# Kernel tuning notes

Hardware: AMD Instinct MI355X
Metric: run time of the kernel (lower is better)

The kernel has to match this reference:

```python
import jax, jax.numpy as jnp
import numpy as np

DIM = 1024
NUM_HEADS = 16
HEAD_DIM = DIM // NUM_HEADS
SCALE = HEAD_DIM ** -0.5


def setup_inputs() -> dict:
    key = jax.random.key(0)
    k1, k2, k3 = jax.random.split(key, 3)
    B, N = 4, 2048
    x = jax.random.normal(k1, (B, N, DIM), dtype=jnp.float32)
    W_qkv = jax.random.normal(k2, (DIM, 3 * DIM), dtype=jnp.float32) * (DIM ** -0.5)
    b_qkv = jnp.zeros((3 * DIM,), dtype=jnp.float32)
    W_proj = jax.random.normal(k3, (DIM, DIM), dtype=jnp.float32) * (DIM ** -0.5)
    b_proj = jnp.zeros((DIM,), dtype=jnp.float32)
    return {"x": x, "W_qkv": W_qkv, "b_qkv": b_qkv, "W_proj": W_proj, "b_proj": b_proj}


def reference(x, W_qkv, b_qkv, W_proj, b_proj):
    B, N, D = x.shape
    qkv = x @ W_qkv + b_qkv                       # [B, N, 3D]
    qkv = qkv.reshape(B, N, 3, NUM_HEADS, HEAD_DIM)
    qkv = jnp.transpose(qkv, (2, 0, 3, 1, 4))     # [3, B, H, N, hd]
    q, k, v = qkv[0], qkv[1], qkv[2]
    attn = jnp.einsum('bhnd,bhmd->bhnm', q, k) * SCALE
    attn = jax.nn.softmax(attn, axis=-1)
    out = jnp.einsum('bhnm,bhmd->bhnd', attn, v)  # [B, H, N, hd]
    out = jnp.transpose(out, (0, 2, 1, 3)).reshape(B, N, D)
    return out @ W_proj + b_proj
```

## Files before the change

kernel.cpp:

```cpp
#include <hip/hip_runtime.h>
#include <hip/hip_bf16.h>

#define BATCH 4
#define SEQ   2048
#define DIM   1024
#define NHEAD 16
#define HDIM  64
#define ROWS  (BATCH * SEQ)
#define LS    68
#define GLS   68
#define QSCALE 0.18033688011f

typedef __bf16 bf16x8 __attribute__((ext_vector_type(8)));
typedef float  f32x4  __attribute__((ext_vector_type(4)));
typedef float  f32x16 __attribute__((ext_vector_type(16)));

static __device__ __forceinline__ uint pack2(float a, float b) {
    ushort ua = __builtin_bit_cast(ushort, (__bf16)a);
    ushort ub = __builtin_bit_cast(ushort, (__bf16)b);
    return (uint)ua | ((uint)ub << 16);
}
#define PLSWAP(a, b) asm volatile("v_permlane32_swap_b32 %0, %1" : "+v"(a), "+v"(b))

__global__ __launch_bounds__(256)
void convert_bf16_kernel(const float* __restrict__ in, ushort* __restrict__ out, int n8) {
    int stride = gridDim.x * blockDim.x;
    for (int i = blockIdx.x * blockDim.x + threadIdx.x; i < n8; i += stride) {
        float4 a = ((const float4*)in)[2 * i];
        float4 b = ((const float4*)in)[2 * i + 1];
        ushort u[8];
        u[0] = __builtin_bit_cast(ushort, (__bf16)a.x);
        u[1] = __builtin_bit_cast(ushort, (__bf16)a.y);
        u[2] = __builtin_bit_cast(ushort, (__bf16)a.z);
        u[3] = __builtin_bit_cast(ushort, (__bf16)a.w);
        u[4] = __builtin_bit_cast(ushort, (__bf16)b.x);
        u[5] = __builtin_bit_cast(ushort, (__bf16)b.y);
        u[6] = __builtin_bit_cast(ushort, (__bf16)b.z);
        u[7] = __builtin_bit_cast(ushort, (__bf16)b.w);
        ((uint4*)out)[i] = *(uint4*)u;
    }
}

__global__ __launch_bounds__(256)
void transpose_bf16_kernel(const float* __restrict__ W, ushort* __restrict__ Wt,
                           int K, int N) {
    __shared__ float tile[32][33];
    const int tx = threadIdx.x, ty = threadIdx.y;
    const int n0 = blockIdx.x * 32, k0 = blockIdx.y * 32;
#pragma unroll
    for (int i = 0; i < 4; ++i)
        tile[ty + 8 * i][tx] = W[(long)(k0 + ty + 8 * i) * N + n0 + tx];
    __syncthreads();
#pragma unroll
    for (int i = 0; i < 4; ++i) {
        float v = tile[tx][ty + 8 * i];
        Wt[(long)(n0 + ty + 8 * i) * K + k0 + tx] = __builtin_bit_cast(ushort, (__bf16)v);
    }
}

__global__ __launch_bounds__(256)
void gemm_mfma_kernel(const ushort* __restrict__ A, const ushort* __restrict__ Bt,
                      const float* __restrict__ bias,
                      int M, int N, int K, int mode,
                      __hip_bfloat16* __restrict__ Qb,
                      __hip_bfloat16* __restrict__ Kb,
                      __hip_bfloat16* __restrict__ Vb,
                      float* __restrict__ Cout) {
    const int t  = threadIdx.x;
    const int w  = t >> 6;
    const int l  = t & 63;
    const int c  = l & 15;
    const int g  = l >> 4;
    const int wr = w >> 1, wc = w & 1;
    const int row0 = blockIdx.y * 128;
    const int col0 = blockIdx.x * 128;

    __shared__ ushort As[128][GLS];
    __shared__ ushort Bs[128][GLS];

    const int sr = t >> 3;
    const int sa = t & 7;

    f32x4 acc[4][4];
#pragma unroll
    for (int i = 0; i < 4; ++i)
#pragma unroll
        for (int j = 0; j < 4; ++j) acc[i][j] = (f32x4){0.f, 0.f, 0.f, 0.f};

    for (int k0 = 0; k0 < K; k0 += 64) {
        __syncthreads();
#pragma unroll
        for (int i = 0; i < 4; ++i) {
            int row = i * 32 + sr;
            uint4 a = *(const uint4*)(A + (size_t)(row0 + row) * K + k0 + 8 * sa);
            *(uint2*)&As[row][8 * sa]     = make_uint2(a.x, a.y);
            *(uint2*)&As[row][8 * sa + 4] = make_uint2(a.z, a.w);
            uint4 b = *(const uint4*)(Bt + (size_t)(col0 + row) * K + k0 + 8 * sa);
            *(uint2*)&Bs[row][8 * sa]     = make_uint2(b.x, b.y);
            *(uint2*)&Bs[row][8 * sa + 4] = make_uint2(b.z, b.w);
        }
        __syncthreads();

#pragma unroll
        for (int ks = 0; ks < 2; ++ks) {
            bf16x8 am[4], bn[4];
#pragma unroll
            for (int mt = 0; mt < 4; ++mt) {
                uint2 a0 = *(const uint2*)&As[wr * 64 + mt * 16 + c][ks * 32 + 8 * g];
                uint2 a1 = *(const uint2*)&As[wr * 64 + mt * 16 + c][ks * 32 + 8 * g + 4];
                am[mt] = __builtin_bit_cast(bf16x8, make_uint4(a0.x, a0.y, a1.x, a1.y));
            }
#pragma unroll
            for (int nt = 0; nt < 4; ++nt) {
                uint2 b0 = *(const uint2*)&Bs[wc * 64 + nt * 16 + c][ks * 32 + 8 * g];
                uint2 b1 = *(const uint2*)&Bs[wc * 64 + nt * 16 + c][ks * 32 + 8 * g + 4];
                bn[nt] = __builtin_bit_cast(bf16x8, make_uint4(b0.x, b0.y, b1.x, b1.y));
            }
#pragma unroll
            for (int mt = 0; mt < 4; ++mt)
#pragma unroll
                for (int nt = 0; nt < 4; ++nt)
                    acc[mt][nt] = __builtin_amdgcn_mfma_f32_16x16x32_bf16(
                        am[mt], bn[nt], acc[mt][nt], 0, 0, 0);
        }
    }

    float bv[4];
#pragma unroll
    for (int nt = 0; nt < 4; ++nt) bv[nt] = bias[col0 + wc * 64 + nt * 16 + c];

#pragma unroll
    for (int mt = 0; mt < 4; ++mt) {
#pragma unroll
        for (int r = 0; r < 4; ++r) {
            int grow = row0 + wr * 64 + mt * 16 + 4 * g + r;
#pragma unroll
            for (int nt = 0; nt < 4; ++nt) {
                int gcol = col0 + wc * 64 + nt * 16 + c;
                float v = acc[mt][nt][r] + bv[nt];
                if (mode == 0) {
                    int s = gcol >> 10;
                    int hc = gcol & 1023;
                    int h = hc >> 6, d = hc & 63;
                    int bi = grow >> 11, n = grow & 2047;
                    size_t off = ((size_t)(bi * NHEAD + h) * SEQ + n) * HDIM + d;
                    if (s == 0) v *= QSCALE;
                    __hip_bfloat16 hb = __float2bfloat16(v);
                    if (s == 0)      Qb[off] = hb;
                    else if (s == 1) Kb[off] = hb;
                    else             Vb[off] = hb;
                } else {
                    Cout[(size_t)grow * N + gcol] = v;
                }
            }
        }
    }
}

__global__ __launch_bounds__(256)
void attn_mfma2_kernel(const ushort* __restrict__ Qg,
                       const ushort* __restrict__ Kg,
                       const ushort* __restrict__ Vg,
                       ushort* __restrict__ O) {
    const int id  = blockIdx.x;
    const int bh  = (id & 7) * 8 + ((id >> 3) & 7);
    const int qt  = id >> 6;
    const int t   = threadIdx.x;
    const int w   = t >> 6, l = t & 63;
    const int lo5 = l & 31, hi = l >> 5;
    const size_t base = (size_t)bh * SEQ * HDIM;
    const int q0  = qt * 128 + w * 32;

    __shared__ ushort Ks[2][64 * LS];
    __shared__ ushort Vt[2][64 * LS];

    bf16x8 qf[4];
    {
        const ushort* qrow = Qg + base + (size_t)(q0 + lo5) * HDIM + 8 * hi;
#pragma unroll
        for (int db = 0; db < 4; ++db)
            qf[db] = __builtin_bit_cast(bf16x8, *(const uint4*)(qrow + 16 * db));
    }

    const int ksr = t & 63, kch = t >> 6;
    const int vkp = t & 31, vcg = t >> 5;
    const ushort* Kptr = Kg + base + (size_t)ksr * HDIM + 16 * kch;
    const ushort* Vptr = Vg + base + (size_t)(2 * vkp) * HDIM + 8 * vcg;

    auto stageK = [&](int buf, uint4 a, uint4 b) {
        ushort* p = &Ks[buf][ksr * LS + 16 * kch];
        *(uint2*)(p)      = make_uint2(a.x, a.y);
        *(uint2*)(p + 4)  = make_uint2(a.z, a.w);
        *(uint2*)(p + 8)  = make_uint2(b.x, b.y);
        *(uint2*)(p + 12) = make_uint2(b.z, b.w);
    };
    auto stageV = [&](int buf, uint4 a, uint4 b) {
        const uint* pa = (const uint*)&a;
        const uint* pb = (const uint*)&b;
#pragma unroll
        for (int e = 0; e < 8; ++e) {
            uint sel = (e & 1) ? 0x07060302u : 0x05040100u;
            uint packed = __builtin_amdgcn_perm(pb[e >> 1], pa[e >> 1], sel);
            *(uint*)&Vt[buf][(8 * vcg + e) * LS + 2 * vkp] = packed;
        }
    };

    uint4 kr0, kr1, vr0, vr1;
    kr0 = *(const uint4*)(Kptr);
    kr1 = *(const uint4*)(Kptr + 8);
    vr0 = *(const uint4*)(Vptr);
    vr1 = *(const uint4*)(Vptr + HDIM);
    stageK(0, kr0, kr1);
    stageV(0, vr0, vr1);
    {
        const size_t off = (size_t)64 * HDIM;
        kr0 = *(const uint4*)(Kptr + off);
        kr1 = *(const uint4*)(Kptr + off + 8);
        vr0 = *(const uint4*)(Vptr + off);
        vr1 = *(const uint4*)(Vptr + off + HDIM);
    }
    __syncthreads();

    f32x16 o0, o1;
#pragma unroll
    for (int r = 0; r < 16; ++r) { o0[r] = 0.f; o1[r] = 0.f; }
    float m0 = -1e30f, ll = 0.f;

    for (int kt = 0; kt < 32; ++kt) {
        const int cur = kt & 1;
        if (kt < 31) {
            stageK(cur ^ 1, kr0, kr1);
            stageV(cur ^ 1, vr0, vr1);
        }
        if (kt < 30) {
            const size_t off = (size_t)(kt + 2) * 64 * HDIM;
            kr0 = *(const uint4*)(Kptr + off);
            kr1 = *(const uint4*)(Kptr + off + 8);
            vr0 = *(const uint4*)(Vptr + off);
            vr1 = *(const uint4*)(Vptr + off + HDIM);
        }

        f32x16 s[2];
        __builtin_amdgcn_s_setprio(1);
#pragma unroll
        for (int kb = 0; kb < 2; ++kb) {
            f32x16 acc;
#pragma unroll
            for (int r = 0; r < 16; ++r) acc[r] = 0.f;
#pragma unroll
            for (int db = 0; db < 4; ++db) {
                const ushort* ap = &Ks[cur][(kb * 32 + lo5) * LS + 16 * db + 8 * hi];
                uint2 a0 = *(const uint2*)(ap);
                uint2 a1 = *(const uint2*)(ap + 4);
                bf16x8 af = __builtin_bit_cast(bf16x8, make_uint4(a0.x, a0.y, a1.x, a1.y));
                acc = __builtin_amdgcn_mfma_f32_32x32x16_bf16(af, qf[db], acc, 0, 0, 0);
            }
            s[kb] = acc;
        }
        __builtin_amdgcn_s_setprio(0);

        float c0 = s[0][0], c1 = s[0][1];
#pragma unroll
        for (int r = 2; r < 16; r += 2) {
            c0 = fmaxf(fmaxf(c0, s[0][r]), s[0][r + 1]);
            c1 = fmaxf(fmaxf(c1, s[1][r]), s[1][r + 1]);
        }
        c0 = fmaxf(fmaxf(c0, s[1][0]), s[1][1]);
        float pmax = fmaxf(c0, c1);
        pmax = fmaxf(pmax, __shfl_xor(pmax, 32, 64));

        if (!__all(pmax <= m0 + 8.f)) {
            float mn = fmaxf(m0, pmax);
            float corr = __builtin_amdgcn_exp2f(m0 - mn);
#pragma unroll
            for (int r = 0; r < 16; ++r) { o0[r] *= corr; o1[r] *= corr; }
            ll *= corr;
            m0 = mn;
        }
        float a0 = 0.f, a1 = 0.f, a2 = 0.f, a3 = 0.f;
#pragma unroll
        for (int r = 0; r < 16; r += 2) {
            float p0 = __builtin_amdgcn_exp2f(s[0][r]     - m0); s[0][r]     = p0; a0 += p0;
            float p1 = __builtin_amdgcn_exp2f(s[0][r + 1] - m0); s[0][r + 1] = p1; a1 += p1;
            float p2 = __builtin_amdgcn_exp2f(s[1][r]     - m0); s[1][r]     = p2; a2 += p2;
            float p3 = __builtin_amdgcn_exp2f(s[1][r + 1] - m0); s[1][r + 1] = p3; a3 += p3;
        }
        float rs = (a0 + a1) + (a2 + a3);
        rs += __shfl_xor(rs, 32, 64);
        ll += rs;

        bf16x8 pbf[4];
#pragma unroll
        for (int kb = 0; kb < 2; ++kb)
#pragma unroll
            for (int kk = 0; kk < 2; ++kk) {
                const int b0 = kk * 8;
                uint w0 = pack2(s[kb][b0 + 0], s[kb][b0 + 1]);
                uint w1 = pack2(s[kb][b0 + 2], s[kb][b0 + 3]);
                uint w2 = pack2(s[kb][b0 + 4], s[kb][b0 + 5]);
                uint w3 = pack2(s[kb][b0 + 6], s[kb][b0 + 7]);
                PLSWAP(w0, w2);
                PLSWAP(w1, w3);
                pbf[kb * 2 + kk] = __builtin_bit_cast(bf16x8, make_uint4(w0, w1, w2, w3));
            }

        __builtin_amdgcn_s_setprio(1);
#pragma unroll
        for (int kb = 0; kb < 2; ++kb)
#pragma unroll
            for (int kk = 0; kk < 2; ++kk) {
                const int kcol = kb * 32 + kk * 16 + 8 * hi;
                const ushort* vp0 = &Vt[cur][lo5 * LS + kcol];
                uint2 v0 = *(const uint2*)(vp0);
                uint2 v1 = *(const uint2*)(vp0 + 4);
                bf16x8 vf0 = __builtin_bit_cast(bf16x8, make_uint4(v0.x, v0.y, v1.x, v1.y));
                o0 = __builtin_amdgcn_mfma_f32_32x32x16_bf16(vf0, pbf[kb * 2 + kk], o0, 0, 0, 0);
                const ushort* vp1 = vp0 + 32 * LS;
                uint2 v2 = *(const uint2*)(vp1);
                uint2 v3 = *(const uint2*)(vp1 + 4);
                bf16x8 vf1 = __builtin_bit_cast(bf16x8, make_uint4(v2.x, v2.y, v3.x, v3.y));
                o1 = __builtin_amdgcn_mfma_f32_32x32x16_bf16(vf1, pbf[kb * 2 + kk], o1, 0, 0, 0);
            }
        __builtin_amdgcn_s_setprio(0);

        __syncthreads();
    }

    const float inv = 1.f / ll;
    const int b = bh >> 4, h = bh & 15;
    ushort* orow = O + (size_t)(b * SEQ + q0 + lo5) * DIM + h * HDIM;
#pragma unroll
    for (int j = 0; j < 4; ++j) {
        uint2 st;
        st.x = pack2(o0[4 * j + 0] * inv, o0[4 * j + 1] * inv);
        st.y = pack2(o0[4 * j + 2] * inv, o0[4 * j + 3] * inv);
        *(uint2*)(orow + 8 * j + 4 * hi) = st;
        st.x = pack2(o1[4 * j + 0] * inv, o1[4 * j + 1] * inv);
        st.y = pack2(o1[4 * j + 2] * inv, o1[4 * j + 3] * inv);
        *(uint2*)(orow + 32 + 8 * j + 4 * hi) = st;
    }
}

extern "C" void kernel_launch(void* const* d_in, const int* in_sizes, int n_in,
                              void* d_out, int out_size, void* d_ws, size_t ws_size,
                              hipStream_t stream) {
    const float* x      = (const float*)d_in[0];
    const float* W_qkv  = (const float*)d_in[1];
    const float* b_qkv  = (const float*)d_in[2];
    const float* W_proj = (const float*)d_in[3];
    const float* b_proj = (const float*)d_in[4];
    float* out = (float*)d_out;

    const size_t qkv_elems = (size_t)BATCH * NHEAD * SEQ * HDIM;
    char* ws = (char*)d_ws;
    ushort* xb      = (ushort*)ws;
    ushort* Wqkv_t  = (ushort*)(ws + qkv_elems * 2);
    ushort* Wproj_t = (ushort*)(ws + qkv_elems * 2 + (size_t)DIM * 3 * DIM * 2);
    char*   ws2     = ws + qkv_elems * 2 + (size_t)DIM * 3 * DIM * 2 + (size_t)DIM * DIM * 2;
    __hip_bfloat16* Qb = (__hip_bfloat16*)ws2;
    __hip_bfloat16* Kb = (__hip_bfloat16*)(ws2 + qkv_elems * 2);
    __hip_bfloat16* Vb = (__hip_bfloat16*)(ws2 + qkv_elems * 4);
    ushort* attnout = xb;

    convert_bf16_kernel<<<2048, 256, 0, stream>>>(x, xb, ROWS * DIM / 8);
    transpose_bf16_kernel<<<dim3(3 * DIM / 32, DIM / 32), dim3(32, 8), 0, stream>>>(
        W_qkv, Wqkv_t, DIM, 3 * DIM);
    transpose_bf16_kernel<<<dim3(DIM / 32, DIM / 32), dim3(32, 8), 0, stream>>>(
        W_proj, Wproj_t, DIM, DIM);

    gemm_mfma_kernel<<<dim3(3 * DIM / 128, ROWS / 128), 256, 0, stream>>>(
        xb, Wqkv_t, b_qkv, ROWS, 3 * DIM, DIM, 0, Qb, Kb, Vb, nullptr);

    attn_mfma2_kernel<<<dim3(1024), 256, 0, stream>>>(
        (const ushort*)Qb, (const ushort*)Kb, (const ushort*)Vb, attnout);

    gemm_mfma_kernel<<<dim3(DIM / 128, ROWS / 128), 256, 0, stream>>>(
        attnout, Wproj_t, b_proj, ROWS, DIM, DIM, 1, nullptr, nullptr, nullptr, out);
}
```

Before: 239.0 us.

## Double attention query tile per block and split K/V staging across warps

```diff
diff --git a/kernel.cpp b/kernel.cpp
--- a/kernel.cpp
+++ b/kernel.cpp
@@ -7,7 +7,7 @@
 #define NHEAD 16
 #define HDIM  64
 #define ROWS  (BATCH * SEQ)
-#define LS    68
+#define LS    72
 #define GLS   68
 #define QSCALE 0.18033688011f
 
@@ -157,7 +157,7 @@
     }
 }
 
-__global__ __launch_bounds__(256)
+__global__ __launch_bounds__(512)
 void attn_mfma2_kernel(const ushort* __restrict__ Qg,
                        const ushort* __restrict__ Kg,
                        const ushort* __restrict__ Vg,
@@ -169,7 +169,7 @@
     const int w   = t >> 6, l = t & 63;
     const int lo5 = l & 31, hi = l >> 5;
     const size_t base = (size_t)bh * SEQ * HDIM;
-    const int q0  = qt * 128 + w * 32;
+    const int q0  = qt * 256 + w * 32;
 
     __shared__ ushort Ks[2][64 * LS];
     __shared__ ushort Vt[2][64 * LS];
@@ -182,42 +182,39 @@
             qf[db] = __builtin_bit_cast(bf16x8, *(const uint4*)(qrow + 16 * db));
     }
 
-    const int ksr = t & 63, kch = t >> 6;
-    const int vkp = t & 31, vcg = t >> 5;
-    const ushort* Kptr = Kg + base + (size_t)ksr * HDIM + 16 * kch;
-    const ushort* Vptr = Vg + base + (size_t)(2 * vkp) * HDIM + 8 * vcg;
-
-    auto stageK = [&](int buf, uint4 a, uint4 b) {
-        ushort* p = &Ks[buf][ksr * LS + 16 * kch];
-        *(uint2*)(p)      = make_uint2(a.x, a.y);
-        *(uint2*)(p + 4)  = make_uint2(a.z, a.w);
-        *(uint2*)(p + 8)  = make_uint2(b.x, b.y);
-        *(uint2*)(p + 12) = make_uint2(b.z, b.w);
+    const bool isV = (t < 256);
+    const int vkp = t & 31, vcg = (t >> 5) & 7;
+    const int u   = t & 255;
+    const int ksr = u & 63, kch = u >> 6;
+    const ushort* gptr = isV
+        ? (Vg + base + (size_t)(2 * vkp) * HDIM + 8 * vcg)
+        : (Kg + base + (size_t)ksr * HDIM + 16 * kch);
+    const int second = isV ? HDIM : 8;
+
+    auto stage = [&](int buf, uint4 a, uint4 b) {
+        if (isV) {
+            const uint* pa = (const uint*)&a;
+            const uint* pb = (const uint*)&b;
+#pragma unroll
+            for (int e = 0; e < 8; ++e) {
+                uint sel = (e & 1) ? 0x07060302u : 0x05040100u;
+                uint packed = __builtin_amdgcn_perm(pb[e >> 1], pa[e >> 1], sel);
+                *(uint*)&Vt[buf][(8 * vcg + e) * LS + 2 * vkp] = packed;
+            }
+        } else {
+            ushort* p = &Ks[buf][ksr * LS + 16 * kch];
+            *(uint4*)(p)     = a;
+            *(uint4*)(p + 8) = b;
+        }
     };
-    auto stageV = [&](int buf, uint4 a, uint4 b) {
-        const uint* pa = (const uint*)&a;
-        const uint* pb = (const uint*)&b;
-#pragma unroll
-        for (int e = 0; e < 8; ++e) {
-            uint sel = (e & 1) ? 0x07060302u : 0x05040100u;
-            uint packed = __builtin_amdgcn_perm(pb[e >> 1], pa[e >> 1], sel);
-            *(uint*)&Vt[buf][(8 * vcg + e) * LS + 2 * vkp] = packed;
-        }
-    };
-
-    uint4 kr0, kr1, vr0, vr1;
-    kr0 = *(const uint4*)(Kptr);
-    kr1 = *(const uint4*)(Kptr + 8);
-    vr0 = *(const uint4*)(Vptr);
-    vr1 = *(const uint4*)(Vptr + HDIM);
-    stageK(0, kr0, kr1);
-    stageV(0, vr0, vr1);
+
+    uint4 r0 = *(const uint4*)(gptr);
+    uint4 r1 = *(const uint4*)(gptr + second);
+    stage(0, r0, r1);
     {
         const size_t off = (size_t)64 * HDIM;
-        kr0 = *(const uint4*)(Kptr + off);
-        kr1 = *(const uint4*)(Kptr + off + 8);
-        vr0 = *(const uint4*)(Vptr + off);
-        vr1 = *(const uint4*)(Vptr + off + HDIM);
+        r0 = *(const uint4*)(gptr + off);
+        r1 = *(const uint4*)(gptr + off + second);
     }
     __syncthreads();
 
@@ -228,16 +225,11 @@
 
     for (int kt = 0; kt < 32; ++kt) {
         const int cur = kt & 1;
-        if (kt < 31) {
-            stageK(cur ^ 1, kr0, kr1);
-            stageV(cur ^ 1, vr0, vr1);
-        }
+        if (kt < 31) stage(cur ^ 1, r0, r1);
         if (kt < 30) {
             const size_t off = (size_t)(kt + 2) * 64 * HDIM;
-            kr0 = *(const uint4*)(Kptr + off);
-            kr1 = *(const uint4*)(Kptr + off + 8);
-            vr0 = *(const uint4*)(Vptr + off);
-            vr1 = *(const uint4*)(Vptr + off + HDIM);
+            r0 = *(const uint4*)(gptr + off);
+            r1 = *(const uint4*)(gptr + off + second);
         }
 
         f32x16 s[2];
@@ -249,10 +241,8 @@
             for (int r = 0; r < 16; ++r) acc[r] = 0.f;
 #pragma unroll
             for (int db = 0; db < 4; ++db) {
-                const ushort* ap = &Ks[cur][(kb * 32 + lo5) * LS + 16 * db + 8 * hi];
-                uint2 a0 = *(const uint2*)(ap);
-                uint2 a1 = *(const uint2*)(ap + 4);
-                bf16x8 af = __builtin_bit_cast(bf16x8, make_uint4(a0.x, a0.y, a1.x, a1.y));
+                uint4 araw = *(const uint4*)&Ks[cur][(kb * 32 + lo5) * LS + 16 * db + 8 * hi];
+                bf16x8 af = __builtin_bit_cast(bf16x8, araw);
                 acc = __builtin_amdgcn_mfma_f32_32x32x16_bf16(af, qf[db], acc, 0, 0, 0);
             }
             s[kb] = acc;
@@ -310,15 +300,11 @@
 #pragma unroll
             for (int kk = 0; kk < 2; ++kk) {
                 const int kcol = kb * 32 + kk * 16 + 8 * hi;
-                const ushort* vp0 = &Vt[cur][lo5 * LS + kcol];
-                uint2 v0 = *(const uint2*)(vp0);
-                uint2 v1 = *(const uint2*)(vp0 + 4);
-                bf16x8 vf0 = __builtin_bit_cast(bf16x8, make_uint4(v0.x, v0.y, v1.x, v1.y));
+                uint4 vraw0 = *(const uint4*)&Vt[cur][lo5 * LS + kcol];
+                bf16x8 vf0 = __builtin_bit_cast(bf16x8, vraw0);
                 o0 = __builtin_amdgcn_mfma_f32_32x32x16_bf16(vf0, pbf[kb * 2 + kk], o0, 0, 0, 0);
-                const ushort* vp1 = vp0 + 32 * LS;
-                uint2 v2 = *(const uint2*)(vp1);
-                uint2 v3 = *(const uint2*)(vp1 + 4);
-                bf16x8 vf1 = __builtin_bit_cast(bf16x8, make_uint4(v2.x, v2.y, v3.x, v3.y));
+                uint4 vraw1 = *(const uint4*)&Vt[cur][(lo5 + 32) * LS + kcol];
+                bf16x8 vf1 = __builtin_bit_cast(bf16x8, vraw1);
                 o1 = __builtin_amdgcn_mfma_f32_32x32x16_bf16(vf1, pbf[kb * 2 + kk], o1, 0, 0, 0);
             }
         __builtin_amdgcn_s_setprio(0);
@@ -371,7 +357,7 @@
     gemm_mfma_kernel<<<dim3(3 * DIM / 128, ROWS / 128), 256, 0, stream>>>(
         xb, Wqkv_t, b_qkv, ROWS, 3 * DIM, DIM, 0, Qb, Kb, Vb, nullptr);
 
-    attn_mfma2_kernel<<<dim3(1024), 256, 0, stream>>>(
+    attn_mfma2_kernel<<<dim3(512), 512, 0, stream>>>(
         (const ushort*)Qb, (const ushort*)Kb, (const ushort*)Vb, attnout);
 
     gemm_mfma_kernel<<<dim3(DIM / 128, ROWS / 128), 256, 0, stream>>>(
```

Measured after the change: 223.1 us. 6.7% less time.
